# Optimization experiments

Hardware: AMD Instinct MI355X
Metric: run time of the kernel (lower is better)

The kernel has to match this reference:

```python
import jax, jax.numpy as jnp
import numpy as np

B, CIN, C, H, W = 4, 256, 128, 64, 64
LN_EPS = 1e-5


def _conv1x1(x, Wk, bk):
    # x: [B, Cin, H, W], Wk: [Cout, Cin] -> [B, Cout, H, W]
    return jnp.einsum('bchw,oc->bohw', x, Wk) + bk[None, :, None, None]


def setup_inputs() -> dict:
    key = jax.random.key(0)
    ks = jax.random.split(key, 11)
    s_in = 1.0 / np.sqrt(CIN)
    s_c = 1.0 / np.sqrt(C)
    return {
        'x': jax.random.normal(ks[0], (B, CIN, H, W), jnp.float32),
        'Wg': jax.random.normal(ks[1], (C, CIN), jnp.float32) * s_in,
        'bg': jax.random.normal(ks[2], (C,), jnp.float32) * s_in,
        'Wt': jax.random.normal(ks[3], (C, CIN), jnp.float32) * s_in,
        'bt': jax.random.normal(ks[4], (C,), jnp.float32) * s_in,
        'Wp': jax.random.normal(ks[5], (C, CIN), jnp.float32) * s_in,
        'bp': jax.random.normal(ks[6], (C,), jnp.float32) * s_in,
        'Wz': jax.random.normal(ks[7], (CIN, C), jnp.float32) * s_c,
        'bz': jax.random.normal(ks[8], (CIN,), jnp.float32) * s_c,
        'gamma': jax.random.normal(ks[9], (CIN, H, W), jnp.float32),
        'beta': jax.random.normal(ks[10], (CIN,), jnp.float32).reshape(CIN, 1, 1) * jnp.ones((CIN, H, W), jnp.float32),
    }


def reference(x, Wg, bg, Wt, bt, Wp, bp, Wz, bz, gamma, beta):
    b, cin, h, w = x.shape
    n = h * w
    # 1x1 conv projections -> flatten spatial
    g = _conv1x1(x, Wg, bg).reshape(b, C, n).transpose(0, 2, 1)      # [B, N, C]
    theta = _conv1x1(x, Wt, bt).reshape(b, C, n).transpose(0, 2, 1)  # [B, N, C]
    phi = _conv1x1(x, Wp, bp).reshape(b, C, n)                        # [B, C, N]
    # embedded-gaussian attention: no scaling, softmax over keys
    f = jnp.einsum('bnc,bcm->bnm', theta, phi)                        # [B, N, N]
    attn = jax.nn.softmax(f, axis=-1)
    y = jnp.einsum('bnm,bmc->bnc', attn, g)                           # [B, N, C]
    y = y.transpose(0, 2, 1).reshape(b, C, h, w)                      # [B, C, H, W]
    # output projection + LayerNorm over [Cin, H, W]
    z = _conv1x1(y, Wz, bz)                                           # [B, Cin, H, W]
    mean = jnp.mean(z, axis=(1, 2, 3), keepdims=True)
    var = jnp.var(z, axis=(1, 2, 3), keepdims=True)
    ln = (z - mean) * jax.lax.rsqrt(var + LN_EPS) * gamma[None] + beta[None]
    return ln + x
```

## Files before the change

### kernel.cpp

```cpp
#include <hip/hip_runtime.h>
#include <hip/hip_bf16.h>


#define BB   4
#define CINC 256
#define CCH  128
#define NS   4096
#define LN_EPS 1e-5f

typedef unsigned short ushort_t;
typedef unsigned int   uint_t;
typedef __bf16 bf16x8 __attribute__((ext_vector_type(8)));
typedef float  f32x4  __attribute__((ext_vector_type(4)));
typedef float  f32x16 __attribute__((ext_vector_type(16)));

typedef const __attribute__((address_space(1))) void* gas_ptr;
typedef __attribute__((address_space(3))) void*       las_ptr;

__device__ __forceinline__ void gload16(const ushort_t* g, ushort_t* l) {
    __builtin_amdgcn_global_load_lds((gas_ptr)g, (las_ptr)l, 16, 0, 0);
}

__device__ __forceinline__ float4 ld4(const float* p) { return *reinterpret_cast<const float4*>(p); }
__device__ __forceinline__ void   st4(float* p, float4 v) { *reinterpret_cast<float4*>(p) = v; }

__device__ __forceinline__ ushort_t f2bf(float f) {
    __hip_bfloat16 h = __float2bfloat16(f);
    return *reinterpret_cast<ushort_t*>(&h);
}
__device__ __forceinline__ float bf2f(ushort_t u) {
    __hip_bfloat16 h = *reinterpret_cast<__hip_bfloat16*>(&u);
    return __bfloat162float(h);
}
__device__ __forceinline__ uint_t pk2(float a, float b) {
    return (uint_t)f2bf(a) | ((uint_t)f2bf(b) << 16);
}

__device__ __forceinline__ void split8(const float* v, uint_t* hw, uint_t* lw) {
#pragma unroll
    for (int jj = 0; jj < 4; ++jj) {
        ushort_t h0 = f2bf(v[2 * jj]);
        ushort_t h1 = f2bf(v[2 * jj + 1]);
        ushort_t e0 = f2bf(v[2 * jj] - bf2f(h0));
        ushort_t e1 = f2bf(v[2 * jj + 1] - bf2f(h1));
        hw[jj] = (uint_t)h0 | ((uint_t)h1 << 16);
        lw[jj] = (uint_t)e0 | ((uint_t)e1 << 16);
    }
}

__global__ __launch_bounds__(256) void split_kernel(
    const float* __restrict__ x,
    ushort_t* __restrict__ xTh, ushort_t* __restrict__ xTl)
{
    __shared__ float T[64 * 68];

    const int tid = threadIdx.x;
    const int n0  = blockIdx.x * 64;
    const int k0  = blockIdx.y * 64;
    const int b   = blockIdx.z;

#pragma unroll
    for (int u = 0; u < 4; ++u) {
        int fi = u * 256 + tid;
        int k  = fi >> 4;
        int c4 = fi & 15;
        float4 v = ld4(&x[(size_t)(b * CINC + k0 + k) * NS + n0 + c4 * 4]);
        T[(c4 * 4 + 0) * 68 + k] = v.x;
        T[(c4 * 4 + 1) * 68 + k] = v.y;
        T[(c4 * 4 + 2) * 68 + k] = v.z;
        T[(c4 * 4 + 3) * 68 + k] = v.w;
    }
    __syncthreads();

#pragma unroll
    for (int u = 0; u < 2; ++u) {
        int fi = u * 256 + tid;
        int n  = fi >> 3;
        int j  = fi & 7;
        float4 a0 = ld4(&T[n * 68 + j * 8]);
        float4 a1 = ld4(&T[n * 68 + j * 8 + 4]);
        float v[8] = {a0.x, a0.y, a0.z, a0.w, a1.x, a1.y, a1.z, a1.w};
        uint_t hw[4], lw[4];
        split8(v, hw, lw);
        size_t base = (size_t)(b * NS + n0 + n) * CINC + k0 + ((j ^ (n & 7)) * 8);
        *reinterpret_cast<uint4*>(&xTh[base]) = make_uint4(hw[0], hw[1], hw[2], hw[3]);
        *reinterpret_cast<uint4*>(&xTl[base]) = make_uint4(lw[0], lw[1], lw[2], lw[3]);
    }
}

__global__ __launch_bounds__(256) void wsplit_all_kernel(
    const float* __restrict__ Wt, const float* __restrict__ Wp,
    const float* __restrict__ Wg, const float* __restrict__ Wz,
    ushort_t* __restrict__ Whs, ushort_t* __restrict__ Wls,
    ushort_t* __restrict__ Wzh, ushort_t* __restrict__ Wzl)
{
    int task = blockIdx.x * 256 + threadIdx.x;
    if (task < 384 * 32) {
        int o = task >> 5;
        int j = task & 31;
        int mid = o >> 7;
        int r   = o & 127;
        const float* Wsel = (mid == 0) ? Wt : (mid == 1) ? Wp : Wg;
        float4 a0 = ld4(&Wsel[(size_t)r * CINC + j * 8]);
        float4 a1 = ld4(&Wsel[(size_t)r * CINC + j * 8 + 4]);
        float v[8] = {a0.x, a0.y, a0.z, a0.w, a1.x, a1.y, a1.z, a1.w};
        uint_t hw[4], lw[4];
        split8(v, hw, lw);
        int kb = j >> 3, jj8 = j & 7;
        size_t base = (size_t)o * CINC + kb * 64 + ((jj8 ^ (o & 7)) * 8);
        *reinterpret_cast<uint4*>(&Whs[base]) = make_uint4(hw[0], hw[1], hw[2], hw[3]);
        *reinterpret_cast<uint4*>(&Wls[base]) = make_uint4(lw[0], lw[1], lw[2], lw[3]);
    } else {
        int t2 = task - 384 * 32;
        int o = t2 >> 4;
        int j = t2 & 15;
        float4 a0 = ld4(&Wz[(size_t)o * CCH + j * 8]);
        float4 a1 = ld4(&Wz[(size_t)o * CCH + j * 8 + 4]);
        float v[8] = {a0.x, a0.y, a0.z, a0.w, a1.x, a1.y, a1.z, a1.w};
        uint_t hw[4], lw[4];
        split8(v, hw, lw);
        size_t base = (size_t)o * CCH + (j >> 3) * 64 + (((j & 7) ^ (o & 7)) * 8);
        *reinterpret_cast<uint4*>(&Wzh[base]) = make_uint4(hw[0], hw[1], hw[2], hw[3]);
        *reinterpret_cast<uint4*>(&Wzl[base]) = make_uint4(lw[0], lw[1], lw[2], lw[3]);
    }
}

__global__ __launch_bounds__(256) void proj_mfma_kernel(
    const ushort_t* __restrict__ xTh, const ushort_t* __restrict__ xTl,
    const ushort_t* __restrict__ Whs, const ushort_t* __restrict__ Wls,
    const float* __restrict__ bt, const float* __restrict__ bp,
    const float* __restrict__ bg,
    ushort_t* __restrict__ Qhi, ushort_t* __restrict__ Qlo,
    ushort_t* __restrict__ KhiS, ushort_t* __restrict__ KloS,
    ushort_t* __restrict__ VtS)
{
    __shared__ __align__(16) char smem[65536];
    ushort_t* Wh_l = (ushort_t*)smem;
    ushort_t* Wl_l = (ushort_t*)(smem + 16384);
    ushort_t* Xh_l = (ushort_t*)(smem + 32768);
    ushort_t* Xl_l = (ushort_t*)(smem + 49152);
    float*    T    = (float*)smem;

    const int tid  = threadIdx.x;
    const int w    = tid >> 6;
    const int lane = tid & 63;
    const int l31  = lane & 31;
    const int h    = lane >> 5;
    const int n0   = blockIdx.x * 128;
    const int og   = blockIdx.y;
    const int b    = blockIdx.z;

    const float* bsel = (og == 0) ? bt : (og == 1) ? bp : bg;

    f32x16 acc[4];
#pragma unroll
    for (int ng = 0; ng < 4; ++ng)
#pragma unroll
        for (int r = 0; r < 16; ++r) acc[ng][r] = 0.f;

    const int ol   = w * 32 + l31;
    const int swzq = l31 & 7;

    for (int kb = 0; kb < 4; ++kb) {
        if (kb > 0) __syncthreads();
#pragma unroll
        for (int p = 0; p < 4; ++p) {
            int e  = p * 2048 + tid * 8;
            int rr = e >> 6;
            int kk = e & 63;
            gload16(Whs + (size_t)(og * 128 + rr) * CINC + kb * 64 + kk, Wh_l + e);
            gload16(Wls + (size_t)(og * 128 + rr) * CINC + kb * 64 + kk, Wl_l + e);
            gload16(xTh + (size_t)(b * NS + n0 + rr) * CINC + kb * 64 + kk, Xh_l + e);
            gload16(xTl + (size_t)(b * NS + n0 + rr) * CINC + kb * 64 + kk, Xl_l + e);
        }
        __syncthreads();

        __builtin_amdgcn_s_setprio(1);
#pragma unroll
        for (int k16 = 0; k16 < 4; ++k16) {
            int c8  = k16 * 2 + h;
            int swz = c8 ^ swzq;
            bf16x8 ah = *reinterpret_cast<const bf16x8*>(&Wh_l[ol * 64 + swz * 8]);
            bf16x8 al = *reinterpret_cast<const bf16x8*>(&Wl_l[ol * 64 + swz * 8]);
#pragma unroll
            for (int ng = 0; ng < 4; ++ng) {
                int nl = ng * 32 + l31;
                bf16x8 xh = *reinterpret_cast<const bf16x8*>(&Xh_l[nl * 64 + swz * 8]);
                bf16x8 xl = *reinterpret_cast<const bf16x8*>(&Xl_l[nl * 64 + swz * 8]);
                acc[ng] = __builtin_amdgcn_mfma_f32_32x32x16_bf16(ah, xh, acc[ng], 0, 0, 0);
                acc[ng] = __builtin_amdgcn_mfma_f32_32x32x16_bf16(ah, xl, acc[ng], 0, 0, 0);
                acc[ng] = __builtin_amdgcn_mfma_f32_32x32x16_bf16(al, xh, acc[ng], 0, 0, 0);
            }
        }
        __builtin_amdgcn_s_setprio(0);
    }

    float bv[16];
#pragma unroll
    for (int r = 0; r < 16; ++r)
        bv[r] = bsel[w * 32 + (r & 3) + 8 * (r >> 2) + 4 * h];

    __syncthreads();

    if (og < 2) {
        ushort_t* H = (og == 0) ? Qhi : KhiS;
        ushort_t* L = (og == 0) ? Qlo : KloS;
#pragma unroll
        for (int pass = 0; pass < 2; ++pass) {
#pragma unroll
            for (int ngh = 0; ngh < 2; ++ngh) {
                int ng = pass * 2 + ngh;
                int nl = ngh * 32 + l31;
#pragma unroll
                for (int r = 0; r < 16; ++r) {
                    int o_in = w * 32 + (r & 3) + 8 * (r >> 2) + 4 * h;
                    T[nl * 132 + o_in] = acc[ng][r] + bv[r];
                }
            }
            __syncthreads();
#pragma unroll
            for (int u = 0; u < 4; ++u) {
                int fi = u * 256 + tid;
                int n  = fi >> 4;
                int j  = fi & 15;
                float4 a0 = ld4(&T[n * 132 + j * 8]);
                float4 a1 = ld4(&T[n * 132 + j * 8 + 4]);
                float v[8] = {a0.x, a0.y, a0.z, a0.w, a1.x, a1.y, a1.z, a1.w};
                uint_t hw[4], lw[4];
                split8(v, hw, lw);
                int n_glob = n0 + pass * 64 + n;
                int idx = (og == 1) ? ((j & 8) | ((j & 7) ^ (n & 7))) : j;
                size_t base = (size_t)(b * NS + n_glob) * CCH + idx * 8;
                *reinterpret_cast<uint4*>(&H[base]) = make_uint4(hw[0], hw[1], hw[2], hw[3]);
                *reinterpret_cast<uint4*>(&L[base]) = make_uint4(lw[0], lw[1], lw[2], lw[3]);
            }
            __syncthreads();
        }
    } else {
#pragma unroll
        for (int pass = 0; pass < 2; ++pass) {
            if ((w >> 1) == pass) {
#pragma unroll
                for (int ng = 0; ng < 4; ++ng) {
                    int nl = ng * 32 + l31;
#pragma unroll
                    for (int r = 0; r < 16; ++r) {
                        int c_loc = (w & 1) * 32 + (r & 3) + 8 * (r >> 2) + 4 * h;
                        T[c_loc * 132 + nl] = acc[ng][r] + bv[r];
                    }
                }
            }
            __syncthreads();
#pragma unroll
            for (int u = 0; u < 4; ++u) {
                int fi = u * 256 + tid;
                int c_loc = fi >> 4;
                int nj    = fi & 15;
                float4 a0 = ld4(&T[c_loc * 132 + nj * 8]);
                float4 a1 = ld4(&T[c_loc * 132 + nj * 8 + 4]);
                int c = pass * 64 + c_loc;
                uint4 wv;
                wv.x = pk2(a0.x, a0.y);
                wv.y = pk2(a0.z, a0.w);
                wv.z = pk2(a1.x, a1.y);
                wv.w = pk2(a1.z, a1.w);
                size_t base = (size_t)(b * CCH + c) * NS + n0 + (nj >> 3) * 64
                            + (((nj & 7) ^ (c & 7)) * 8);
                *reinterpret_cast<uint4*>(&VtS[base]) = wv;
            }
            __syncthreads();
        }
    }
}

__global__ __launch_bounds__(512, 2) void attn_kernel(
    const ushort_t* __restrict__ Qhi, const ushort_t* __restrict__ Qlo,
    const ushort_t* __restrict__ KhiS, const ushort_t* __restrict__ KloS,
    const ushort_t* __restrict__ VtS, float* __restrict__ Yp,
    float* __restrict__ ML, int NT)
{
    __shared__ __align__(16) char smem[98304];

    const int tid  = threadIdx.x;
    const int w    = tid >> 6;
    const int lane = tid & 63;
    const int l31  = lane & 31;
    const int h    = lane >> 5;

    int qx, sp, b;
    {
        int lin = (blockIdx.z * gridDim.y + blockIdx.y) * gridDim.x + blockIdx.x;
        if (gridDim.x * gridDim.y * gridDim.z == 256) {
            int xcd  = lin & 7;
            int idx  = lin >> 3;
            int pair = xcd * 2 + (idx >> 4);
            qx = idx & 15;
            b  = pair >> 2;
            sp = pair & 3;
        } else {
            qx = blockIdx.x; sp = blockIdx.y; b = blockIdx.z;
        }
    }
    const int n0 = qx * 256;

    bf16x8 qh[8], ql[8];
    {
        const ushort_t* qrh = Qhi + (size_t)(b * NS + n0 + w * 32 + l31) * CCH;
        const ushort_t* qrl = Qlo + (size_t)(b * NS + n0 + w * 32 + l31) * CCH;
#pragma unroll
        for (int cst = 0; cst < 8; ++cst) {
            qh[cst] = *reinterpret_cast<const bf16x8*>(qrh + cst * 16 + h * 8);
            ql[cst] = *reinterpret_cast<const bf16x8*>(qrl + cst * 16 + h * 8);
        }
    }

    f32x16 yacc[4];
#pragma unroll
    for (int cb = 0; cb < 4; ++cb)
#pragma unroll
        for (int r = 0; r < 16; ++r) yacc[cb][r] = 0.f;
    float m_run = -1e30f, l_run = 0.f;

    const ushort_t* Khg = KhiS + (size_t)b * NS * CCH;
    const ushort_t* Klg = KloS + (size_t)b * NS * CCH;
    const ushort_t* Vtg = VtS + (size_t)b * CCH * NS;

    const int ktbase = sp * NT;

    auto gload_tile = [&](int ktg, int bi) {
        ushort_t* kh = (ushort_t*)(smem + bi * 16384);
        ushort_t* kl = (ushort_t*)(smem + 32768 + bi * 16384);
        ushort_t* vb = (ushort_t*)(smem + 65536 + bi * 16384);
        const size_t koff = (size_t)ktg * 8192;
        const int m0 = ktg * 64;
#pragma unroll
        for (int i = 0; i < 2; ++i) {
            int off = i * 4096 + tid * 8;
            gload16(Khg + koff + off, kh + off);
            gload16(Klg + koff + off, kl + off);
            int cr = off >> 6;
            int cw = off & 63;
            gload16(Vtg + (size_t)cr * NS + m0 + cw, vb + off);
        }
    };

    gload_tile(ktbase, 0);
    __syncthreads();

    const int swzq = l31 & 7;

    for (int kt = 0; kt < NT; ++kt) {
        const int cur = kt & 1;
        const bool more = (kt + 1 < NT);
        if (more) gload_tile(ktbase + kt + 1, cur ^ 1);

        const ushort_t* Kh = (const ushort_t*)(smem + cur * 16384);
        const ushort_t* Kl = (const ushort_t*)(smem + 32768 + cur * 16384);
        const ushort_t* Vl = (const ushort_t*)(smem + 65536 + cur * 16384);

        f32x16 sacc[2];
#pragma unroll
        for (int k2 = 0; k2 < 2; ++k2)
#pragma unroll
            for (int r = 0; r < 16; ++r) sacc[k2][r] = 0.f;

        __builtin_amdgcn_s_setprio(1);
#pragma unroll
        for (int cst = 0; cst < 8; ++cst) {
            int cc  = cst * 2 + h;
            int swz = (cc & 8) | ((cc & 7) ^ swzq);
#pragma unroll
            for (int k2 = 0; k2 < 2; ++k2) {
                int addr = (k2 * 32 + l31) * 128 + swz * 8;
                bf16x8 ah = *reinterpret_cast<const bf16x8*>(&Kh[addr]);
                bf16x8 al = *reinterpret_cast<const bf16x8*>(&Kl[addr]);
                sacc[k2] = __builtin_amdgcn_mfma_f32_32x32x16_bf16(ah, qh[cst], sacc[k2], 0, 0, 0);
                sacc[k2] = __builtin_amdgcn_mfma_f32_32x32x16_bf16(al, qh[cst], sacc[k2], 0, 0, 0);
                sacc[k2] = __builtin_amdgcn_mfma_f32_32x32x16_bf16(ah, ql[cst], sacc[k2], 0, 0, 0);
            }
        }
        __builtin_amdgcn_s_setprio(0);

        float mx = sacc[0][0];
#pragma unroll
        for (int r = 1; r < 16; ++r) mx = fmaxf(mx, sacc[0][r]);
#pragma unroll
        for (int r = 0; r < 16; ++r) mx = fmaxf(mx, sacc[1][r]);
        mx = fmaxf(mx, __shfl_xor(mx, 32));

        const bool defer = __all(mx - m_run <= 8.0f);
        float mref, alpha;
        if (defer) { mref = m_run; alpha = 1.0f; }
        else       { mref = fmaxf(m_run, mx); alpha = __expf(m_run - mref); }

        bf16x8 pb[4];
        float psum = 0.f;
#pragma unroll
        for (int k2 = 0; k2 < 2; ++k2) {
            float pe[16];
#pragma unroll
            for (int r = 0; r < 16; ++r) {
                pe[r] = __expf(sacc[k2][r] - mref);
                psum += pe[r];
            }
#pragma unroll
            for (int a = 0; a < 2; ++a) {
                uint_t w0 = pk2(pe[8 * a + 0], pe[8 * a + 1]);
                uint_t w1 = pk2(pe[8 * a + 2], pe[8 * a + 3]);
                uint_t w2 = pk2(pe[8 * a + 4], pe[8 * a + 5]);
                uint_t w3 = pk2(pe[8 * a + 6], pe[8 * a + 7]);
                uint_t s0 = (uint_t)__shfl_xor((int)w0, 32);
                uint_t s1 = (uint_t)__shfl_xor((int)w1, 32);
                uint_t s2 = (uint_t)__shfl_xor((int)w2, 32);
                uint_t s3 = (uint_t)__shfl_xor((int)w3, 32);
                uint_t u0 = h ? s2 : w0;
                uint_t u1 = h ? s3 : w1;
                uint_t u2 = h ? w2 : s0;
                uint_t u3 = h ? w3 : s1;
                uint4 packed = make_uint4(u0, u1, u2, u3);
                pb[k2 * 2 + a] = *reinterpret_cast<bf16x8*>(&packed);
            }
        }
        psum += __shfl_xor(psum, 32);

        if (defer) {
            l_run += psum;
        } else {
            l_run = l_run * alpha + psum;
            m_run = mref;
#pragma unroll
            for (int cb = 0; cb < 4; ++cb)
#pragma unroll
                for (int r = 0; r < 16; ++r) yacc[cb][r] *= alpha;
        }

        __builtin_amdgcn_s_setprio(1);
#pragma unroll
        for (int cb = 0; cb < 4; ++cb) {
            int crow = (cb * 32 + l31) * 64;
#pragma unroll
            for (int ks = 0; ks < 4; ++ks) {
                int kc = ks * 2 + h;
                bf16x8 av = *reinterpret_cast<const bf16x8*>(&Vl[crow + (kc ^ swzq) * 8]);
                yacc[cb] = __builtin_amdgcn_mfma_f32_32x32x16_bf16(av, pb[ks], yacc[cb], 0, 0, 0);
            }
        }
        __builtin_amdgcn_s_setprio(0);

        __syncthreads();
    }

    float* stage = (float*)smem;
    float* Ybase = Yp + ((size_t)(sp * BB + b) * NS + n0) * CCH;
#pragma unroll
    for (int pass = 0; pass < 4; ++pass) {
        if ((w >> 1) == pass) {
            int qrow = (w & 1) * 32 + l31;
#pragma unroll
            for (int cb = 0; cb < 4; ++cb)
#pragma unroll
                for (int r = 0; r < 16; ++r) {
                    int c = cb * 32 + (r & 3) + 8 * (r >> 2) + 4 * h;
                    stage[qrow * 132 + c] = yacc[cb][r];
                }
        }
        __syncthreads();
#pragma unroll
        for (int u = 0; u < 4; ++u) {
            int idx = u * 512 + tid;
            int row = idx >> 5;
            int c4  = idx & 31;
            st4(&Ybase[(size_t)(pass * 64 + row) * CCH + c4 * 4],
                ld4(&stage[row * 132 + c4 * 4]));
        }
        __syncthreads();
    }
    if (h == 0) {
        size_t mi = ((size_t)(sp * BB + b) * NS + n0 + w * 32 + l31) * 2;
        ML[mi + 0] = m_run;
        ML[mi + 1] = l_run;
    }
}

__global__ __launch_bounds__(256) void merge_kernel(
    const float* __restrict__ Yp, const float* __restrict__ ML,
    ushort_t* __restrict__ Ymh, ushort_t* __restrict__ Yml, int nsplit)
{
    const int total = BB * NS * (CCH / 8);
    for (int t = blockIdx.x * 256 + threadIdx.x; t < total;
         t += gridDim.x * 256) {
        int b = t >> 16;
        int r = t & 65535;
        int n = r >> 4;
        int j = r & 15;

        float ms[4], ls[4];
        float m = -1e30f;
#pragma unroll
        for (int s = 0; s < 4; ++s) {
            if (s < nsplit) {
                size_t mi = ((size_t)(s * BB + b) * NS + n) * 2;
                ms[s] = ML[mi + 0];
                ls[s] = ML[mi + 1];
                m = fmaxf(m, ms[s]);
            }
        }
        float den = 0.f;
        float wt[4];
#pragma unroll
        for (int s = 0; s < 4; ++s) {
            if (s < nsplit) {
                wt[s] = __expf(ms[s] - m);
                den += ls[s] * wt[s];
            }
        }
        float inv = 1.0f / den;

        float acc[8] = {0.f, 0.f, 0.f, 0.f, 0.f, 0.f, 0.f, 0.f};
#pragma unroll
        for (int s = 0; s < 4; ++s) {
            if (s < nsplit) {
                float a = wt[s] * inv;
                const float* yr = &Yp[((size_t)(s * BB + b) * NS + n) * CCH + j * 8];
                float4 y0 = ld4(yr);
                float4 y1 = ld4(yr + 4);
                acc[0] += a * y0.x; acc[1] += a * y0.y;
                acc[2] += a * y0.z; acc[3] += a * y0.w;
                acc[4] += a * y1.x; acc[5] += a * y1.y;
                acc[6] += a * y1.z; acc[7] += a * y1.w;
            }
        }
        uint_t hw[4], lw[4];
        split8(acc, hw, lw);
        size_t base = (size_t)(b * NS + n) * CCH + (j >> 3) * 64
                    + (((j & 7) ^ (n & 7)) * 8);
        *reinterpret_cast<uint4*>(&Ymh[base]) = make_uint4(hw[0], hw[1], hw[2], hw[3]);
        *reinterpret_cast<uint4*>(&Yml[base]) = make_uint4(lw[0], lw[1], lw[2], lw[3]);
    }
}

__global__ __launch_bounds__(256) void zgemm_kernel(
    const ushort_t* __restrict__ Ymh, const ushort_t* __restrict__ Yml,
    const ushort_t* __restrict__ Wzh, const ushort_t* __restrict__ Wzl,
    const float* __restrict__ bz, float* __restrict__ Z,
    float* __restrict__ partials)
{
    __shared__ __align__(16) char smem[65536];
    ushort_t* Wh_l = (ushort_t*)smem;
    ushort_t* Wl_l = (ushort_t*)(smem + 16384);
    ushort_t* Yh_l = (ushort_t*)(smem + 32768);
    ushort_t* Yl_l = (ushort_t*)(smem + 49152);
    __shared__ float red[8];

    const int tid  = threadIdx.x;
    const int w    = tid >> 6;
    const int lane = tid & 63;
    const int l31  = lane & 31;
    const int h    = lane >> 5;
    const int n0   = blockIdx.x * 128;
    const int o0   = blockIdx.y * 128;
    const int b    = blockIdx.z;

    f32x16 acc[4];
#pragma unroll
    for (int ng = 0; ng < 4; ++ng)
#pragma unroll
        for (int r = 0; r < 16; ++r) acc[ng][r] = 0.f;

    const int ol   = w * 32 + l31;
    const int swzq = l31 & 7;

    for (int kb = 0; kb < 2; ++kb) {
        if (kb > 0) __syncthreads();
#pragma unroll
        for (int p = 0; p < 4; ++p) {
            int e  = p * 2048 + tid * 8;
            int rr = e >> 6;
            int kk = e & 63;
            gload16(Wzh + (size_t)(o0 + rr) * CCH + kb * 64 + kk, Wh_l + e);
            gload16(Wzl + (size_t)(o0 + rr) * CCH + kb * 64 + kk, Wl_l + e);
            gload16(Ymh + (size_t)(b * NS + n0 + rr) * CCH + kb * 64 + kk, Yh_l + e);
            gload16(Yml + (size_t)(b * NS + n0 + rr) * CCH + kb * 64 + kk, Yl_l + e);
        }
        __syncthreads();

        __builtin_amdgcn_s_setprio(1);
#pragma unroll
        for (int k16 = 0; k16 < 4; ++k16) {
            int c8  = k16 * 2 + h;
            int swz = c8 ^ swzq;
            bf16x8 ah = *reinterpret_cast<const bf16x8*>(&Wh_l[ol * 64 + swz * 8]);
            bf16x8 al = *reinterpret_cast<const bf16x8*>(&Wl_l[ol * 64 + swz * 8]);
#pragma unroll
            for (int ng = 0; ng < 4; ++ng) {
                int nl = ng * 32 + l31;
                bf16x8 yh = *reinterpret_cast<const bf16x8*>(&Yh_l[nl * 64 + swz * 8]);
                bf16x8 yl = *reinterpret_cast<const bf16x8*>(&Yl_l[nl * 64 + swz * 8]);
                acc[ng] = __builtin_amdgcn_mfma_f32_32x32x16_bf16(ah, yh, acc[ng], 0, 0, 0);
                acc[ng] = __builtin_amdgcn_mfma_f32_32x32x16_bf16(ah, yl, acc[ng], 0, 0, 0);
                acc[ng] = __builtin_amdgcn_mfma_f32_32x32x16_bf16(al, yh, acc[ng], 0, 0, 0);
            }
        }
        __builtin_amdgcn_s_setprio(0);
    }

    float s = 0.f, s2 = 0.f;
#pragma unroll
    for (int r = 0; r < 16; ++r) {
        int o = o0 + w * 32 + (r & 3) + 8 * (r >> 2) + 4 * h;
        float bias = bz[o];
        float* zrow = &Z[(size_t)(b * CINC + o) * NS + n0 + l31];
#pragma unroll
        for (int ng = 0; ng < 4; ++ng) {
            float v = acc[ng][r] + bias;
            zrow[ng * 32] = v;
            s  += v;
            s2 += v * v;
        }
    }
#pragma unroll
    for (int off = 1; off < 64; off <<= 1) {
        s  += __shfl_xor(s, off);
        s2 += __shfl_xor(s2, off);
    }
    if (lane == 0) { red[w * 2] = s; red[w * 2 + 1] = s2; }
    __syncthreads();
    if (tid == 0) {
        float ts  = red[0] + red[2] + red[4] + red[6];
        float ts2 = red[1] + red[3] + red[5] + red[7];
        int pidx = (b * 2 + blockIdx.y) * 32 + blockIdx.x;
        partials[pidx * 2 + 0] = ts;
        partials[pidx * 2 + 1] = ts2;
    }
}

__global__ void ln_stats_kernel(const float* __restrict__ partials,
                                float* __restrict__ stats)
{
    const int b = blockIdx.x;
    const int t = threadIdx.x;
    float s  = partials[(size_t)(b * 64 + t) * 2 + 0];
    float s2 = partials[(size_t)(b * 64 + t) * 2 + 1];
#pragma unroll
    for (int off = 1; off < 64; off <<= 1) {
        s  += __shfl_xor(s, off);
        s2 += __shfl_xor(s2, off);
    }
    if (t == 0) {
        const float M = 1048576.f;
        float mean = s / M;
        float var  = s2 / M - mean * mean;
        stats[b * 2 + 0] = mean;
        stats[b * 2 + 1] = rsqrtf(var + LN_EPS);
    }
}

__global__ __launch_bounds__(256) void final_kernel(
    const float* __restrict__ Z, const float* __restrict__ x,
    const float* __restrict__ gamma, const float* __restrict__ beta,
    const float* __restrict__ stats, float* __restrict__ out)
{
    const int total4 = BB * CINC * NS / 4;
    for (int i4 = blockIdx.x * 256 + threadIdx.x; i4 < total4;
         i4 += gridDim.x * 256) {
        int b  = i4 >> 18;
        int r4 = i4 & ((1 << 18) - 1);
        float mean = stats[b * 2 + 0];
        float rstd = stats[b * 2 + 1];
        float4 zv = ld4(&Z[(size_t)i4 * 4]);
        float4 xv = ld4(&x[(size_t)i4 * 4]);
        float4 gv = ld4(&gamma[(size_t)r4 * 4]);
        float4 bv = ld4(&beta[(size_t)r4 * 4]);
        float4 o;
        o.x = (zv.x - mean) * rstd * gv.x + bv.x + xv.x;
        o.y = (zv.y - mean) * rstd * gv.y + bv.y + xv.y;
        o.z = (zv.z - mean) * rstd * gv.z + bv.z + xv.z;
        o.w = (zv.w - mean) * rstd * gv.w + bv.w + xv.w;
        st4(&out[(size_t)i4 * 4], o);
    }
}

extern "C" void kernel_launch(void* const* d_in, const int* in_sizes, int n_in,
                              void* d_out, int out_size, void* d_ws, size_t ws_size,
                              hipStream_t stream)
{
    const float* x     = (const float*)d_in[0];
    const float* Wg    = (const float*)d_in[1];
    const float* bg    = (const float*)d_in[2];
    const float* Wt    = (const float*)d_in[3];
    const float* bt    = (const float*)d_in[4];
    const float* Wp    = (const float*)d_in[5];
    const float* bp    = (const float*)d_in[6];
    const float* Wz    = (const float*)d_in[7];
    const float* bz    = (const float*)d_in[8];
    const float* gamma = (const float*)d_in[9];
    const float* beta  = (const float*)d_in[10];
    float* out = (float*)d_out;

    const size_t SZH = (size_t)BB * NS * CCH * sizeof(ushort_t);
    const size_t WZB = (size_t)CINC * CCH * sizeof(ushort_t);
    const size_t need4 = 5 * SZH
                       + (size_t)4 * BB * NS * CCH * sizeof(float)
                       + (size_t)4 * BB * NS * 2 * sizeof(float)
                       + (size_t)BB * 64 * 2 * sizeof(float)
                       + 2 * WZB + 512;
    const int nsplit = (ws_size >= need4) ? 4 : 2;
    const int NT = (NS / 64) / nsplit;

    char* p = (char*)d_ws;
    ushort_t* Qhi  = (ushort_t*)p; p += SZH;
    ushort_t* Qlo  = (ushort_t*)p; p += SZH;
    ushort_t* KhiS = (ushort_t*)p; p += SZH;
    ushort_t* KloS = (ushort_t*)p; p += SZH;
    ushort_t* VtS  = (ushort_t*)p; p += SZH;
    float* Yp = (float*)p; p += (size_t)nsplit * BB * NS * CCH * sizeof(float);
    float* ML = (float*)p; p += (size_t)nsplit * BB * NS * 2 * sizeof(float);
    float* partials = (float*)p; p += BB * 64 * 2 * sizeof(float);
    float* stats    = (float*)p; p += 64;
    ushort_t* Wzh = (ushort_t*)p; p += WZB;
    ushort_t* Wzl = (ushort_t*)p;

    ushort_t* Ymh = (ushort_t*)Qhi;
    ushort_t* Yml = (ushort_t*)Qlo;
    float*    Z   = (float*)Yp;

    ushort_t* xTh = (ushort_t*)Yp;
    ushort_t* xTl = xTh + (size_t)BB * NS * CINC;
    ushort_t* Whs = (ushort_t*)((char*)Yp + 2 * (size_t)BB * NS * CINC * 2);
    ushort_t* Wls = Whs + (size_t)384 * CINC;

    split_kernel<<<dim3(NS / 64, CINC / 64, BB), 256, 0, stream>>>(x, xTh, xTl);
    wsplit_all_kernel<<<dim3(64), 256, 0, stream>>>(Wt, Wp, Wg, Wz,
                                                    Whs, Wls, Wzh, Wzl);
    proj_mfma_kernel<<<dim3(NS / 128, 3, BB), 256, 0, stream>>>(
        xTh, xTl, Whs, Wls, bt, bp, bg, Qhi, Qlo, KhiS, KloS, VtS);
    attn_kernel<<<dim3(NS / 256, nsplit, BB), 512, 0, stream>>>(
        Qhi, Qlo, KhiS, KloS, VtS, Yp, ML, NT);
    merge_kernel<<<dim3(1024), 256, 0, stream>>>(Yp, ML, Ymh, Yml, nsplit);
    zgemm_kernel<<<dim3(NS / 128, 2, BB), 256, 0, stream>>>(
        Ymh, Yml, Wzh, Wzl, bz, Z, partials);
    ln_stats_kernel<<<dim3(BB), 64, 0, stream>>>(partials, stats);
    final_kernel<<<dim3(2048), 256, 0, stream>>>(Z, x, gamma, beta, stats, out);
}
```

Before: 129.4 us.

## Software-pipeline attention loop so QK of next tile overlaps softmax and PV

Splits the attention loop into separate QK, softmax/pack and PV stages. The QK scores for tile k+1 are computed in the same step as softmax and PV for tile k, using ping-pong score registers, so the matrix units stay busy while the exponentials run. V tiles get a third LDS buffer, which raises shared memory from 96KB to 112KB. The extra score accumulators add register pressure that may cause spills. The loop epilogue assumes an even tile count of at least 2.

```diff
diff --git a/kernel.cpp b/kernel.cpp
--- a/kernel.cpp
+++ b/kernel.cpp
@@ -279,7 +279,7 @@
     const ushort_t* __restrict__ VtS, float* __restrict__ Yp,
     float* __restrict__ ML, int NT)
 {
-    __shared__ __align__(16) char smem[98304];
+    __shared__ __align__(16) char smem[114688];
 
     const int tid  = threadIdx.x;
     const int w    = tid >> 6;
@@ -320,51 +320,46 @@
 #pragma unroll
         for (int r = 0; r < 16; ++r) yacc[cb][r] = 0.f;
     float m_run = -1e30f, l_run = 0.f;
+    f32x16 sA[2], sB[2];
+    bf16x8 pb[4];
 
     const ushort_t* Khg = KhiS + (size_t)b * NS * CCH;
     const ushort_t* Klg = KloS + (size_t)b * NS * CCH;
     const ushort_t* Vtg = VtS + (size_t)b * CCH * NS;
 
     const int ktbase = sp * NT;
-
-    auto gload_tile = [&](int ktg, int bi) {
+    const int swzq = l31 & 7;
+
+    auto gload_k = [&](int ktg, int bi) {
         ushort_t* kh = (ushort_t*)(smem + bi * 16384);
         ushort_t* kl = (ushort_t*)(smem + 32768 + bi * 16384);
-        ushort_t* vb = (ushort_t*)(smem + 65536 + bi * 16384);
         const size_t koff = (size_t)ktg * 8192;
-        const int m0 = ktg * 64;
 #pragma unroll
         for (int i = 0; i < 2; ++i) {
             int off = i * 4096 + tid * 8;
             gload16(Khg + koff + off, kh + off);
             gload16(Klg + koff + off, kl + off);
+        }
+    };
+    auto gload_v = [&](int ktg, int vi) {
+        ushort_t* vb = (ushort_t*)(smem + 65536 + vi * 16384);
+        const int m0 = ktg * 64;
+#pragma unroll
+        for (int i = 0; i < 2; ++i) {
+            int off = i * 4096 + tid * 8;
             int cr = off >> 6;
             int cw = off & 63;
             gload16(Vtg + (size_t)cr * NS + m0 + cw, vb + off);
         }
     };
 
-    gload_tile(ktbase, 0);
-    __syncthreads();
-
-    const int swzq = l31 & 7;
-
-    for (int kt = 0; kt < NT; ++kt) {
-        const int cur = kt & 1;
-        const bool more = (kt + 1 < NT);
-        if (more) gload_tile(ktbase + kt + 1, cur ^ 1);
-
-        const ushort_t* Kh = (const ushort_t*)(smem + cur * 16384);
-        const ushort_t* Kl = (const ushort_t*)(smem + 32768 + cur * 16384);
-        const ushort_t* Vl = (const ushort_t*)(smem + 65536 + cur * 16384);
-
-        f32x16 sacc[2];
+    auto qk = [&](int bi, f32x16 (&s)[2]) {
+        const ushort_t* Kh = (const ushort_t*)(smem + bi * 16384);
+        const ushort_t* Kl = (const ushort_t*)(smem + 32768 + bi * 16384);
 #pragma unroll
         for (int k2 = 0; k2 < 2; ++k2)
 #pragma unroll
-            for (int r = 0; r < 16; ++r) sacc[k2][r] = 0.f;
-
-        __builtin_amdgcn_s_setprio(1);
+            for (int r = 0; r < 16; ++r) s[k2][r] = 0.f;
 #pragma unroll
         for (int cst = 0; cst < 8; ++cst) {
             int cc  = cst * 2 + h;
@@ -374,18 +369,19 @@
                 int addr = (k2 * 32 + l31) * 128 + swz * 8;
                 bf16x8 ah = *reinterpret_cast<const bf16x8*>(&Kh[addr]);
                 bf16x8 al = *reinterpret_cast<const bf16x8*>(&Kl[addr]);
-                sacc[k2] = __builtin_amdgcn_mfma_f32_32x32x16_bf16(ah, qh[cst], sacc[k2], 0, 0, 0);
-                sacc[k2] = __builtin_amdgcn_mfma_f32_32x32x16_bf16(al, qh[cst], sacc[k2], 0, 0, 0);
-                sacc[k2] = __builtin_amdgcn_mfma_f32_32x32x16_bf16(ah, ql[cst], sacc[k2], 0, 0, 0);
-            }
-        }
-        __builtin_amdgcn_s_setprio(0);
-
-        float mx = sacc[0][0];
-#pragma unroll
-        for (int r = 1; r < 16; ++r) mx = fmaxf(mx, sacc[0][r]);
-#pragma unroll
-        for (int r = 0; r < 16; ++r) mx = fmaxf(mx, sacc[1][r]);
+                s[k2] = __builtin_amdgcn_mfma_f32_32x32x16_bf16(ah, qh[cst], s[k2], 0, 0, 0);
+                s[k2] = __builtin_amdgcn_mfma_f32_32x32x16_bf16(al, qh[cst], s[k2], 0, 0, 0);
+                s[k2] = __builtin_amdgcn_mfma_f32_32x32x16_bf16(ah, ql[cst], s[k2], 0, 0, 0);
+            }
+        }
+    };
+
+    auto softmax_pack = [&](f32x16 (&s)[2]) {
+        float mx = s[0][0];
+#pragma unroll
+        for (int r = 1; r < 16; ++r) mx = fmaxf(mx, s[0][r]);
+#pragma unroll
+        for (int r = 0; r < 16; ++r) mx = fmaxf(mx, s[1][r]);
         mx = fmaxf(mx, __shfl_xor(mx, 32));
 
         const bool defer = __all(mx - m_run <= 8.0f);
@@ -393,14 +389,13 @@
         if (defer) { mref = m_run; alpha = 1.0f; }
         else       { mref = fmaxf(m_run, mx); alpha = __expf(m_run - mref); }
 
-        bf16x8 pb[4];
         float psum = 0.f;
 #pragma unroll
         for (int k2 = 0; k2 < 2; ++k2) {
             float pe[16];
 #pragma unroll
             for (int r = 0; r < 16; ++r) {
-                pe[r] = __expf(sacc[k2][r] - mref);
+                pe[r] = __expf(s[k2][r] - mref);
                 psum += pe[r];
             }
 #pragma unroll
@@ -433,8 +428,10 @@
 #pragma unroll
                 for (int r = 0; r < 16; ++r) yacc[cb][r] *= alpha;
         }
-
-        __builtin_amdgcn_s_setprio(1);
+    };
+
+    auto pv = [&](int vi) {
+        const ushort_t* Vl = (const ushort_t*)(smem + 65536 + vi * 16384);
 #pragma unroll
         for (int cb = 0; cb < 4; ++cb) {
             int crow = (cb * 32 + l31) * 64;
@@ -445,10 +442,51 @@
                 yacc[cb] = __builtin_amdgcn_mfma_f32_32x32x16_bf16(av, pb[ks], yacc[cb], 0, 0, 0);
             }
         }
+    };
+
+    gload_k(ktbase, 0);
+    gload_v(ktbase, 0);
+    __syncthreads();
+
+    if (NT > 1) { gload_k(ktbase + 1, 1); gload_v(ktbase + 1, 1); }
+    __builtin_amdgcn_s_setprio(1);
+    qk(0, sA);
+    __builtin_amdgcn_s_setprio(0);
+    __syncthreads();
+
+    int kt = 1;
+    for (; kt + 1 < NT; kt += 2) {
+        gload_k(ktbase + kt + 1, (kt + 1) & 1);
+        gload_v(ktbase + kt + 1, (kt + 1) % 3);
+        __builtin_amdgcn_s_setprio(1);
+        qk(kt & 1, sB);
+        softmax_pack(sA);
+        pv((kt - 1) % 3);
         __builtin_amdgcn_s_setprio(0);
-
         __syncthreads();
-    }
+
+        if (kt + 2 < NT) {
+            gload_k(ktbase + kt + 2, (kt + 2) & 1);
+            gload_v(ktbase + kt + 2, (kt + 2) % 3);
+        }
+        __builtin_amdgcn_s_setprio(1);
+        qk((kt + 1) & 1, sA);
+        softmax_pack(sB);
+        pv(kt % 3);
+        __builtin_amdgcn_s_setprio(0);
+        __syncthreads();
+    }
+
+    __builtin_amdgcn_s_setprio(1);
+    qk((NT - 1) & 1, sB);
+    softmax_pack(sA);
+    pv((NT - 2) % 3);
+    __builtin_amdgcn_s_setprio(0);
+    softmax_pack(sB);
+    __builtin_amdgcn_s_setprio(1);
+    pv((NT - 1) % 3);
+    __builtin_amdgcn_s_setprio(0);
+    __syncthreads();
 
     float* stage = (float*)smem;
     float* Ybase = Yp + ((size_t)(sp * BB + b) * NS + n0) * CCH;
```

New measurement: 131.3 us. Within noise of the previous version (+1.5%).
